# Kernel optimization log

Hardware: AMD Instinct MI355X
Metric: run time of the kernel (lower is better)

The kernel has to match this reference:

```python
import jax, jax.numpy as jnp
import numpy as np

RATIO = 10.0
MAXPOOL_K = 101   # local-max window (samples)
MED_K = 6000      # MAD window (samples)
MED_STRIDE = MED_K // 2
TOP_K = 100


def setup_inputs() -> dict:
    key = jax.random.key(0)
    xcorr = jax.random.normal(key, (2, 3, 16, 360000), dtype=jnp.float32)
    return {"xcorr": xcorr}


def _detect(xcorr):
    nb, nc, nx, nt = xcorr.shape
    neg = jnp.finfo(xcorr.dtype).min
    # max_pool2d kernel (1, 101), stride 1, pad (0, 50) -> local sliding max over time
    smax = jax.lax.reduce_window(
        xcorr, neg, jax.lax.max,
        (1, 1, 1, MAXPOOL_K), (1, 1, 1, 1),
        [(0, 0), (0, 0), (0, 0), (MAXPOOL_K // 2, MAXPOOL_K // 2)])
    # reflect-pad right by MED_K then unfold(size=MED_K, stride=MED_STRIDE)
    padded = jnp.pad(xcorr, ((0, 0), (0, 0), (0, 0), (0, MED_K)), mode='reflect')
    nblocks = (nt + MED_K) // MED_STRIDE  # exact by construction
    blocks = padded.reshape(nb, nc, nx, nblocks, MED_STRIDE)
    # each window = two consecutive half-overlapping blocks -> [nb,nc,nx,nw,MED_K]
    windows = jnp.concatenate([blocks[..., :-1, :], blocks[..., 1:, :]], axis=-1)
    mid = (MED_K - 1) // 2  # torch.median returns lower median for even n
    med = jnp.sort(windows, axis=-1)[..., mid]
    mad = jnp.sort(jnp.abs(windows - med[..., None]), axis=-1)[..., mid]  # [nb,nc,nx,nw]
    # bilinear interpolate along time by scale MED_STRIDE (align_corners=False), crop to nt
    in_w = mad.shape[-1]
    pos = (jnp.arange(nt, dtype=jnp.float32) + 0.5) / MED_STRIDE - 0.5
    pos = jnp.maximum(pos, 0.0)
    x0 = jnp.minimum(jnp.floor(pos).astype(jnp.int32), in_w - 1)
    x1 = jnp.minimum(x0 + 1, in_w - 1)
    w = pos - x0.astype(jnp.float32)
    mad_t = mad[..., x0] * (1.0 - w) + mad[..., x1] * w  # [nb,nc,nx,nt]
    # keep local maxima exceeding ratio * MAD, zero the rest, then top-k per trace
    keep = (smax == xcorr) & (xcorr > RATIO * mad_t)
    masked = xcorr * keep.astype(xcorr.dtype)
    topk_scores, topk_inds = jax.lax.top_k(masked, TOP_K)
    return topk_scores, topk_inds


def reference(xcorr):
    return _detect(xcorr)
```

## Files before the change

### kernel.cpp

```cpp
#include <hip/hip_runtime.h>
#include <stdint.h>

#define NT      360000
#define NTRACE  96
#define MEDK    6000
#define MSTRIDE 3000
#define NW      121
#define HALFW   50
#define TOPK    100
#define DETCAP  128
#define RATIO_F 10.0f
#define DCHUNKS 12

__device__ __forceinline__ uint32_t f2key(float f) {
    uint32_t u = __float_as_uint(f);
    return (u & 0x80000000u) ? ~u : (u | 0x80000000u);
}
__device__ __forceinline__ float key2f(uint32_t k) {
    uint32_t u = (k & 0x80000000u) ? (k & 0x7fffffffu) : ~k;
    return __uint_as_float(u);
}

struct SelShared {
    uint32_t hist[1024];
    uint32_t scan_a[256];
    uint32_t scan_b[256];
    uint32_t s_bin, s_rank;
};

__device__ float radix_select6000(const float* ls, float sub, bool useabs,
                                  SelShared* sh)
{
    const int tid = threadIdx.x;
    const int wv  = tid >> 6;
    uint32_t prefix = 0, pmask = 0, rank = 3000;
    for (int pass = 0; pass < 4; ++pass) {
        const int shift = 24 - 8 * pass;
        for (int i = tid; i < 1024; i += 256) sh->hist[i] = 0;
        __syncthreads();
        for (int i = tid; i < MEDK; i += 256) {
            float v = ls[i];
            if (useabs) v = fabsf(v - sub);
            uint32_t k = f2key(v);
            if ((k & pmask) == prefix)
                atomicAdd(&sh->hist[wv * 256 + ((k >> shift) & 0xFFu)], 1u);
        }
        __syncthreads();
        uint32_t c = sh->hist[tid] + sh->hist[256 + tid] +
                     sh->hist[512 + tid] + sh->hist[768 + tid];
        sh->scan_a[tid] = c;
        __syncthreads();
        uint32_t* src = sh->scan_a;
        uint32_t* dst = sh->scan_b;
        for (int off = 1; off < 256; off <<= 1) {
            uint32_t v = src[tid];
            if (tid >= off) v += src[tid - off];
            dst[tid] = v;
            __syncthreads();
            uint32_t* t = src; src = dst; dst = t;
        }
        uint32_t incl = src[tid];
        uint32_t excl = incl - c;
        if (incl >= rank && excl < rank) {
            sh->s_bin  = (uint32_t)tid;
            sh->s_rank = rank - excl;
        }
        __syncthreads();
        prefix |= sh->s_bin << shift;
        pmask  |= 0xFFu << shift;
        rank    = sh->s_rank;
        __syncthreads();
    }
    return key2f(prefix);
}

__global__ __launch_bounds__(256) void mad_kernel(const float* __restrict__ x,
                                                  float* __restrict__ mad)
{
    __shared__ float    ls[MEDK];
    __shared__ SelShared sh;
    const int tr = blockIdx.x / NW;
    const int w  = blockIdx.x % NW;
    const float* xt = x + (size_t)tr * NT;
    const int t0 = w * MSTRIDE;
    if (t0 + MEDK <= NT) {
        const float4* src4 = (const float4*)(xt + t0);
        float4* dst4 = (float4*)ls;
        for (int i = threadIdx.x; i < MEDK / 4; i += 256) dst4[i] = src4[i];
    } else {
        for (int i = threadIdx.x; i < MEDK; i += 256) {
            int g = t0 + i;
            int src = (g < NT) ? g : (2 * NT - 2 - g);
            ls[i] = xt[src];
        }
    }
    __syncthreads();
    float med  = radix_select6000(ls, 0.0f, false, &sh);
    __syncthreads();
    float madv = radix_select6000(ls, med,  true,  &sh);
    if (threadIdx.x == 0) mad[tr * NW + w] = madv;
}

__global__ __launch_bounds__(256) void detect_kernel(const float* __restrict__ x,
                                                     const float* __restrict__ mad,
                                                     uint32_t* __restrict__ counters,
                                                     uint64_t* __restrict__ det)
{
    __shared__ float smad[NW];
    const int tr = blockIdx.x / DCHUNKS;
    const int ch = blockIdx.x % DCHUNKS;
    const float* xt = x + (size_t)tr * NT;
    for (int i = threadIdx.x; i < NW; i += 256) smad[i] = mad[tr * NW + i];
    __syncthreads();
    const int tbeg = ch * (NT / DCHUNKS);
    const int tend = tbeg + (NT / DCHUNKS);
    for (int t = tbeg + threadIdx.x * 4; t < tend; t += 256 * 4) {
        float4 v4 = *(const float4*)(xt + t);
        float vv[4] = {v4.x, v4.y, v4.z, v4.w};
        #pragma unroll
        for (int k = 0; k < 4; ++k) {
            int   tt = t + k;
            float v  = vv[k];
            float pos = ((float)tt + 0.5f) / (float)MSTRIDE - 0.5f;
            pos = fmaxf(pos, 0.0f);
            int   x0 = min((int)floorf(pos), NW - 1);
            int   x1 = min(x0 + 1, NW - 1);
            float wg = pos - (float)x0;
            float m  = smad[x0] * (1.0f - wg) + smad[x1] * wg;
            if (v > RATIO_F * m) {
                bool ismax = true;
                int lo = max(tt - HALFW, 0), hi = min(tt + HALFW, NT - 1);
                for (int j = lo; j <= hi && ismax; ++j) ismax = (xt[j] <= v);
                if (ismax) {
                    uint32_t slot = atomicAdd(&counters[tr], 1u);
                    if (slot < DETCAP)
                        det[(size_t)tr * DETCAP + slot] =
                            ((uint64_t)f2key(v) << 32) | (uint32_t)(~(uint32_t)tt);
                }
            }
        }
    }
}

__global__ __launch_bounds__(64) void finalize_kernel(const float* __restrict__ x,
                                                      const uint32_t* __restrict__ counters,
                                                      const uint64_t* __restrict__ det,
                                                      float* __restrict__ out)
{
    __shared__ uint64_t sdet[DETCAP];
    __shared__ int sposs[TOPK];
    __shared__ int snegs[TOPK];
    __shared__ int s_np, s_nn;
    const int tr   = blockIdx.x;
    const int lane = threadIdx.x;
    const int D = (int)min(counters[tr], (uint32_t)DETCAP);
    for (int i = lane; i < D; i += 64) sdet[i] = det[(size_t)tr * DETCAP + i];
    if (lane == 0) { s_np = 0; s_nn = 0; }
    __syncthreads();

    const float* xt = x + (size_t)tr * NT;
    for (int base = 0; base < NT; base += 64) {
        int np0 = s_np, nn0 = s_nn;
        if (np0 >= TOPK && nn0 >= TOPK) break;
        int  t     = base + lane;
        bool valid = (t < NT);
        uint32_t bits = valid ? __float_as_uint(xt[t]) : 0u;
        bool nonneg = valid && !(bits >> 31);
        bool neg    = valid &&  (bits >> 31);
        if (nonneg && D > 0) {
            for (int i = 0; i < D; ++i) {
                int dt = (int)(~(uint32_t)(sdet[i] & 0xFFFFFFFFull));
                if (dt == t) { nonneg = false; break; }
            }
        }
        unsigned long long bp = __ballot(nonneg);
        unsigned long long bn = __ballot(neg);
        unsigned long long below = (1ull << lane) - 1ull;
        int pidx = np0 + __popcll(bp & below);
        int nidx = nn0 + __popcll(bn & below);
        if (nonneg && pidx < TOPK) sposs[pidx] = t;
        if (neg    && nidx < TOPK) snegs[nidx] = t;
        __syncthreads();
        if (lane == 0) { s_np = np0 + __popcll(bp); s_nn = nn0 + __popcll(bn); }
        __syncthreads();
    }
    __syncthreads();

    if (lane == 0) {
        for (int i = 1; i < D; ++i) {
            uint64_t k = sdet[i]; int j = i - 1;
            while (j >= 0 && sdet[j] < k) { sdet[j + 1] = sdet[j]; --j; }
            sdet[j + 1] = k;
        }
    }
    __syncthreads();

    const int nd   = min(D, TOPK);
    const int npos = min(s_np, TOPK);
    float* oscore = out + (size_t)tr * TOPK;
    float* oidx   = out + (size_t)NTRACE * TOPK + (size_t)tr * TOPK;
    for (int j = lane; j < TOPK; j += 64) {
        float sc; int idx;
        if (j < nd) {
            uint64_t k = sdet[j];
            sc  = key2f((uint32_t)(k >> 32));
            idx = (int)(~(uint32_t)(k & 0xFFFFFFFFull));
        } else if (j - nd < npos) {
            sc = 0.0f;  idx = sposs[j - nd];
        } else {
            int jj = j - nd - npos;
            sc = -0.0f; idx = (jj < TOPK) ? snegs[jj] : 0;
        }
        oscore[j] = sc;
        oidx[j]   = (float)idx;
    }
}

extern "C" void kernel_launch(void* const* d_in, const int* in_sizes, int n_in,
                              void* d_out, int out_size, void* d_ws, size_t ws_size,
                              hipStream_t stream)
{
    const float* x = (const float*)d_in[0];
    float* out = (float*)d_out;
    char* ws = (char*)d_ws;
    float*    mad      = (float*)ws;
    uint32_t* counters = (uint32_t*)(ws + 46464);
    uint64_t* det      = (uint64_t*)(ws + 46464 + 384);

    hipMemsetAsync(counters, 0, NTRACE * sizeof(uint32_t), stream);
    hipLaunchKernelGGL(mad_kernel,    dim3(NTRACE * NW),      dim3(256), 0, stream, x, mad);
    hipLaunchKernelGGL(detect_kernel, dim3(NTRACE * DCHUNKS), dim3(256), 0, stream, x, mad, counters, det);
    hipLaunchKernelGGL(finalize_kernel, dim3(NTRACE),         dim3(64),  0, stream, x, counters, det, out);
}
```

Baseline: 607.3 us.

## Compact candidate keys after first radix pass and use wave-shuffle scan

```diff
diff --git a/kernel.cpp b/kernel.cpp
--- a/kernel.cpp
+++ b/kernel.cpp
@@ -11,10 +11,11 @@
 #define DETCAP  128
 #define RATIO_F 10.0f
 #define DCHUNKS 12
+#define CAP     2304
 
 __device__ __forceinline__ uint32_t f2key(float f) {
     uint32_t u = __float_as_uint(f);
-    return (u & 0x80000000u) ? ~u : (u | 0x80000000u);
+    return u ^ (uint32_t)(((int32_t)u >> 31) | 0x80000000);
 }
 __device__ __forceinline__ float key2f(uint32_t k) {
     uint32_t u = (k & 0x80000000u) ? (k & 0x7fffffffu) : ~k;
@@ -23,49 +24,108 @@
 
 struct SelShared {
     uint32_t hist[1024];
-    uint32_t scan_a[256];
-    uint32_t scan_b[256];
-    uint32_t s_bin, s_rank;
+    uint32_t cmp[CAP];
+    uint32_t segtot[4];
+    uint32_t s_bin, s_rank, s_cnt, ccount;
 };
 
-__device__ float radix_select6000(const float* ls, float sub, bool useabs,
-                                  SelShared* sh)
+__device__ void bin_select(SelShared* sh, uint32_t rank)
+{
+    const int tid  = threadIdx.x;
+    const int lane = tid & 63;
+    const int wv   = tid >> 6;
+    uint32_t c = sh->hist[tid] + sh->hist[256 + tid] +
+                 sh->hist[512 + tid] + sh->hist[768 + tid];
+    uint32_t incl = c;
+    #pragma unroll
+    for (int off = 1; off < 64; off <<= 1) {
+        uint32_t v = __shfl_up(incl, off);
+        if (lane >= off) incl += v;
+    }
+    if (lane == 63) sh->segtot[wv] = incl;
+    __syncthreads();
+    uint32_t segoff = 0;
+    for (int j = 0; j < wv; ++j) segoff += sh->segtot[j];
+    incl += segoff;
+    uint32_t excl = incl - c;
+    if (rank > excl && rank <= incl) {
+        sh->s_bin = (uint32_t)tid; sh->s_rank = rank - excl; sh->s_cnt = c;
+    }
+    __syncthreads();
+}
+
+__device__ float select_rank3000(const float* ls, float sub, bool useabs,
+                                 SelShared* sh)
 {
     const int tid = threadIdx.x;
     const int wv  = tid >> 6;
-    uint32_t prefix = 0, pmask = 0, rank = 3000;
-    for (int pass = 0; pass < 4; ++pass) {
+    uint32_t* myhist = &sh->hist[wv * 256];
+
+    for (int i = tid; i < 1024; i += 256) sh->hist[i] = 0;
+    if (tid == 0) sh->ccount = 0;
+    __syncthreads();
+    for (int i = tid; i < MEDK / 4; i += 256) {
+        float4 v4 = ((const float4*)ls)[i];
+        float vv[4] = {v4.x, v4.y, v4.z, v4.w};
+        #pragma unroll
+        for (int e = 0; e < 4; ++e) {
+            float v = vv[e];
+            if (useabs) v = fabsf(v - sub);
+            atomicAdd(&myhist[f2key(v) >> 24], 1u);
+        }
+    }
+    __syncthreads();
+    bin_select(sh, 3000u);
+    const uint32_t b0 = sh->s_bin, cnt = sh->s_cnt;
+    uint32_t rank   = sh->s_rank;
+    uint32_t prefix = b0 << 24;
+    uint32_t pmask  = 0xFF000000u;
+    const bool usec = (cnt <= CAP);
+
+    if (usec) {
+        for (int i = tid; i < MEDK / 4; i += 256) {
+            float4 v4 = ((const float4*)ls)[i];
+            float vv[4] = {v4.x, v4.y, v4.z, v4.w};
+            #pragma unroll
+            for (int e = 0; e < 4; ++e) {
+                float v = vv[e];
+                if (useabs) v = fabsf(v - sub);
+                uint32_t k = f2key(v);
+                if ((k >> 24) == b0) {
+                    uint32_t p = atomicAdd(&sh->ccount, 1u);
+                    sh->cmp[p] = k;
+                }
+            }
+        }
+        __syncthreads();
+    }
+
+    for (int pass = 1; pass < 4; ++pass) {
         const int shift = 24 - 8 * pass;
         for (int i = tid; i < 1024; i += 256) sh->hist[i] = 0;
         __syncthreads();
-        for (int i = tid; i < MEDK; i += 256) {
-            float v = ls[i];
-            if (useabs) v = fabsf(v - sub);
-            uint32_t k = f2key(v);
-            if ((k & pmask) == prefix)
-                atomicAdd(&sh->hist[wv * 256 + ((k >> shift) & 0xFFu)], 1u);
-        }
-        __syncthreads();
-        uint32_t c = sh->hist[tid] + sh->hist[256 + tid] +
-                     sh->hist[512 + tid] + sh->hist[768 + tid];
-        sh->scan_a[tid] = c;
-        __syncthreads();
-        uint32_t* src = sh->scan_a;
-        uint32_t* dst = sh->scan_b;
-        for (int off = 1; off < 256; off <<= 1) {
-            uint32_t v = src[tid];
-            if (tid >= off) v += src[tid - off];
-            dst[tid] = v;
-            __syncthreads();
-            uint32_t* t = src; src = dst; dst = t;
-        }
-        uint32_t incl = src[tid];
-        uint32_t excl = incl - c;
-        if (incl >= rank && excl < rank) {
-            sh->s_bin  = (uint32_t)tid;
-            sh->s_rank = rank - excl;
-        }
-        __syncthreads();
+        if (usec) {
+            for (int i = tid; i < (int)cnt; i += 256) {
+                uint32_t k = sh->cmp[i];
+                if ((k & pmask) == prefix)
+                    atomicAdd(&myhist[(k >> shift) & 0xFFu], 1u);
+            }
+        } else {
+            for (int i = tid; i < MEDK / 4; i += 256) {
+                float4 v4 = ((const float4*)ls)[i];
+                float vv[4] = {v4.x, v4.y, v4.z, v4.w};
+                #pragma unroll
+                for (int e = 0; e < 4; ++e) {
+                    float v = vv[e];
+                    if (useabs) v = fabsf(v - sub);
+                    uint32_t k = f2key(v);
+                    if ((k & pmask) == prefix)
+                        atomicAdd(&myhist[(k >> shift) & 0xFFu], 1u);
+                }
+            }
+        }
+        __syncthreads();
+        bin_select(sh, rank);
         prefix |= sh->s_bin << shift;
         pmask  |= 0xFFu << shift;
         rank    = sh->s_rank;
@@ -77,7 +137,7 @@
 __global__ __launch_bounds__(256) void mad_kernel(const float* __restrict__ x,
                                                   float* __restrict__ mad)
 {
-    __shared__ float    ls[MEDK];
+    __shared__ float     ls[MEDK];
     __shared__ SelShared sh;
     const int tr = blockIdx.x / NW;
     const int w  = blockIdx.x % NW;
@@ -95,9 +155,9 @@
         }
     }
     __syncthreads();
-    float med  = radix_select6000(ls, 0.0f, false, &sh);
-    __syncthreads();
-    float madv = radix_select6000(ls, med,  true,  &sh);
+    float med  = select_rank3000(ls, 0.0f, false, &sh);
+    __syncthreads();
+    float madv = select_rank3000(ls, med,  true,  &sh);
     if (threadIdx.x == 0) mad[tr * NW + w] = madv;
 }
 
```

Result: faster. 550.4 us (-9.4%).
